# Kernel optimization log

Measured on AMD Instinct MI355X. Metric: run time of the kernel, lower is better.

The kernel has to match this reference:

```python
import jax, jax.numpy as jnp
import numpy as np

# dims: batch, query grid len, key (irregular obs) len, raw features, time-embed dim, heads
B, TQ, TK, F, ET, H = 8, 48, 128, 64, 64, 8
DK = ET // H          # per-head time-embed dim = 8
D = 2 * F             # attention value dim = cat(X, mask) = 128
NEG = -10000.0        # masked_fill constant from the torch code


def setup_inputs() -> dict:
    key = jax.random.key(0)
    ks = jax.random.split(key, 12)
    X = jax.random.normal(ks[0], (B, TK, F), dtype=jnp.float32)
    mask_X = (jax.random.uniform(ks[1], (B, TK, F)) < 0.7).astype(jnp.float32)
    T = jax.random.uniform(ks[2], (B, TK), dtype=jnp.float32) * 48.0
    alpha = jax.random.uniform(ks[3], (B, TQ), dtype=jnp.float32) * 48.0
    s = 0.05
    # time embedding params: linear(1->1) and periodic(1 -> ET-1)
    w_lin = jax.random.normal(ks[4], (1, 1)) * s
    b_lin = jnp.zeros((1,), jnp.float32)
    w_per = jax.random.normal(ks[5], (1, ET - 1)) * s
    b_per = jnp.zeros((ET - 1,), jnp.float32)
    # attention projections (stored as [in, out], i.e. torch weight transposed)
    Wq = jax.random.normal(ks[6], (ET, ET)) * s
    bq = jnp.zeros((ET,), jnp.float32)
    Wk = jax.random.normal(ks[7], (ET, ET)) * s
    bk = jnp.zeros((ET,), jnp.float32)
    Wo = jax.random.normal(ks[8], (H * D, ET)) * s   # nhidden = embed_time = ET
    bo = jnp.zeros((ET,), jnp.float32)
    return {"X": X, "mask_X": mask_X, "T": T, "alpha": alpha,
            "w_lin": w_lin, "b_lin": b_lin, "w_per": w_per, "b_per": b_per,
            "Wq": Wq, "bq": bq, "Wk": Wk, "bk": bk, "Wo": Wo, "bo": bo}


def _time_embed(t, w_lin, b_lin, w_per, b_per):
    # t: [B, L] -> [B, L, ET]; cat(linear(t), sin(periodic(t)))
    t = t[..., None]
    return jnp.concatenate([t @ w_lin + b_lin, jnp.sin(t @ w_per + b_per)], axis=-1)


def reference(X, mask_X, T, alpha, w_lin, b_lin, w_per, b_per,
              Wq, bq, Wk, bk, Wo, bo):
    # mTAND core (eval mode, dropout off)
    keys = _time_embed(T, w_lin, b_lin, w_per, b_per)        # [B, TK, ET]
    query = _time_embed(alpha, w_lin, b_lin, w_per, b_per)   # [B, TQ, ET]
    X_irg = jnp.concatenate([X, mask_X], axis=-1)            # [B, TK, D]
    M = jnp.concatenate([mask_X, mask_X], axis=-1)           # [B, TK, D]

    q = (query @ Wq + bq).reshape(B, TQ, H, DK).transpose(0, 2, 1, 3)  # [B,H,TQ,DK]
    k = (keys @ Wk + bk).reshape(B, TK, H, DK).transpose(0, 2, 1, 3)   # [B,H,TK,DK]

    scores = jnp.einsum('bhqd,bhkd->bhqk', q, k) / (DK ** 0.5)        # [B,H,TQ,TK]
    # expand per value-channel and masked_fill(-10000) where mask == 0
    logits = jnp.where(M[:, None, None, :, :] == 0, NEG, scores[..., None])  # [B,H,TQ,TK,D]
    p_attn = jax.nn.softmax(logits, axis=-2)                            # softmax over TK
    out = jnp.einsum('bhqkd,bkd->bhqd', p_attn, X_irg)                  # [B,H,TQ,D]

    x = out.transpose(0, 2, 1, 3).reshape(B, TQ, H * D)                 # [B,TQ,H*D]
    return x @ Wo + bo                                                  # [B,TQ,ET]
```

## Files before the change

kernel.cpp:

```cpp
#include <hip/hip_runtime.h>
#include <math.h>

#define B   8
#define TQ  48
#define TK  128
#define F   64
#define ET  64
#define H   8
#define DK  8
#define D   128

__global__ __launch_bounds__(256) void embed_proj_kernel(
    const float* __restrict__ T,
    const float* __restrict__ alpha,
    const float* __restrict__ w_lin, const float* __restrict__ b_lin,
    const float* __restrict__ w_per, const float* __restrict__ b_per,
    const float* __restrict__ Wq, const float* __restrict__ bq,
    const float* __restrict__ Wk, const float* __restrict__ bk,
    float* __restrict__ kws,
    float* __restrict__ qws)
{
    __shared__ float es[4][ET];
    const int tid = threadIdx.x;
    const int rl  = tid >> 6;
    const int o   = tid & 63;
    const int row = blockIdx.x * 4 + rl;

    const bool is_key = row < B * TK;
    const float t = is_key ? T[row] : alpha[row - B * TK];

    float e;
    if (o == 0) e = t * w_lin[0] + b_lin[0];
    else        e = sinf(t * w_per[o - 1] + b_per[o - 1]);
    es[rl][o] = e;
    __syncthreads();

    const float* Wp   = is_key ? Wk : Wq;
    const float* bias = is_key ? bk : bq;
    float acc = bias[o];
    #pragma unroll 8
    for (int i = 0; i < ET; ++i)
        acc = fmaf(es[rl][i], Wp[i * ET + o], acc);

    if (is_key) {
        const int b  = row >> 7;
        const int kk = row & 127;
        const int h  = o >> 3;
        const int dk = o & 7;
        kws[((b * H + h) * TK + kk) * DK + dk] = acc;
    } else {
        const int r = row - B * TK;
        qws[r * ET + o] = acc;
    }
}

__global__ __launch_bounds__(512) void attn_kernel(
    const float* __restrict__ X,
    const float* __restrict__ mask,
    const float* __restrict__ kws,
    const float* __restrict__ qws,
    const float* __restrict__ Wo,
    const float* __restrict__ bo,
    float* __restrict__ out)
{
    __shared__ float qs[ET];
    __shared__ float Es[H][TK];
    __shared__ float maxs[H];
    __shared__ float Xs[TK][F];
    __shared__ unsigned long long Mb[TK];
    __shared__ float xs[H * D];
    __shared__ float pden[4][H * F];
    __shared__ float pnum[4][H * F];
    __shared__ float red[32][ET];

    const int tid = threadIdx.x;
    const int b = blockIdx.x / TQ;
    const int q = blockIdx.x % TQ;

    if (tid < ET) qs[tid] = qws[(b * TQ + q) * ET + tid];

    const float4* X4  = (const float4*)(X + b * TK * F);
    float4*       Xs4 = (float4*)&Xs[0][0];
    #pragma unroll
    for (int i = 0; i < 4; ++i)
        Xs4[tid + 512 * i] = X4[tid + 512 * i];

    {
        const int wave = tid >> 6, lane = tid & 63;
        const float* mrow = mask + b * TK * F;
        #pragma unroll 4
        for (int i = 0; i < 16; ++i) {
            const int kk = wave * 16 + i;
            const unsigned long long bal = __ballot(mrow[kk * F + lane] != 0.0f);
            if (lane == 0) Mb[kk] = bal;
        }
    }
    __syncthreads();

    const float4* k4 = (const float4*)(kws + b * H * TK * DK);
    #pragma unroll
    for (int i = 0; i < 2; ++i) {
        const int p = tid + 512 * i;
        const int h = p >> 7, kk = p & 127;
        const float4 a0 = k4[(h * TK + kk) * 2 + 0];
        const float4 a1 = k4[(h * TK + kk) * 2 + 1];
        const float* qh = &qs[h * DK];
        float s = a0.x * qh[0] + a0.y * qh[1] + a0.z * qh[2] + a0.w * qh[3]
                + a1.x * qh[4] + a1.y * qh[5] + a1.z * qh[6] + a1.w * qh[7];
        Es[h][kk] = s * 0.35355339059327373f;
    }
    __syncthreads();

    if (tid < 256) {
        const int h = tid >> 5, j = tid & 31;
        float m = fmaxf(fmaxf(Es[h][j], Es[h][j + 32]),
                        fmaxf(Es[h][j + 64], Es[h][j + 96]));
        #pragma unroll
        for (int dlt = 16; dlt >= 1; dlt >>= 1)
            m = fmaxf(m, __shfl_xor(m, dlt));
        if (j == 0) maxs[h] = m;
    }
    __syncthreads();

    #pragma unroll
    for (int i = 0; i < 2; ++i) {
        const int p = tid + 512 * i;
        const int h = p >> 7, kk = p & 127;
        Es[h][kk] = expf(Es[h][kk] - maxs[h]);
    }
    __syncthreads();

    {
        const int f4 = (tid & 15) * 4;
        const int h  = (tid >> 4) & 7;
        const int ks = tid >> 7;
        const int k0 = ks * 32;
        float d0 = 0, d1 = 0, d2 = 0, d3 = 0;
        float n0 = 0, n1 = 0, n2 = 0, n3 = 0;
        #pragma unroll 8
        for (int i = 0; i < 32; ++i) {
            const int kk = k0 + i;
            const float e  = Es[h][kk];
            const float4 x = *(const float4*)&Xs[kk][f4];
            const unsigned int mb = (unsigned int)(Mb[kk] >> f4);
            const float e0 = (mb & 1u) ? e : 0.0f;
            const float e1 = (mb & 2u) ? e : 0.0f;
            const float e2 = (mb & 4u) ? e : 0.0f;
            const float e3 = (mb & 8u) ? e : 0.0f;
            d0 += e0; d1 += e1; d2 += e2; d3 += e3;
            n0 = fmaf(e0, x.x, n0); n1 = fmaf(e1, x.y, n1);
            n2 = fmaf(e2, x.z, n2); n3 = fmaf(e3, x.w, n3);
        }
        const int base = h * F + f4;
        *(float4*)&pden[ks][base] = make_float4(d0, d1, d2, d3);
        *(float4*)&pnum[ks][base] = make_float4(n0, n1, n2, n3);
    }
    __syncthreads();

    {
        const int h = tid >> 6, f = tid & 63;
        const int idx = h * F + f;
        const float den = pden[0][idx] + pden[1][idx] + pden[2][idx] + pden[3][idx];
        const float num = pnum[0][idx] + pnum[1][idx] + pnum[2][idx] + pnum[3][idx];
        float outX, outM;
        if (den > 0.0f) {
            outX = num / den;
            outM = 1.0f;
        } else {
            float sX = 0.0f;
            for (int kk = 0; kk < TK; ++kk) sX += Xs[kk][f];
            outX = sX * (1.0f / TK);
            outM = 0.0f;
        }
        xs[h * D + f]      = outX;
        xs[h * D + 64 + f] = outM;
    }
    __syncthreads();

    {
        const int e4 = (tid & 15) * 4;
        const int p  = tid >> 4;
        const int j0 = p * 32;
        float ax = 0, ay = 0, az = 0, aw = 0;
        #pragma unroll 8
        for (int i = 0; i < 32; ++i) {
            const int j = j0 + i;
            const float xj = xs[j];
            const float4 w = *(const float4*)&Wo[j * ET + e4];
            ax = fmaf(xj, w.x, ax); ay = fmaf(xj, w.y, ay);
            az = fmaf(xj, w.z, az); aw = fmaf(xj, w.w, aw);
        }
        *(float4*)&red[p][e4] = make_float4(ax, ay, az, aw);
    }
    __syncthreads();
    if (tid < ET) {
        float acc = bo[tid];
        #pragma unroll
        for (int p = 0; p < 32; ++p) acc += red[p][tid];
        out[(b * TQ + q) * ET + tid] = acc;
    }
}

extern "C" void kernel_launch(void* const* d_in, const int* in_sizes, int n_in,
                              void* d_out, int out_size, void* d_ws, size_t ws_size,
                              hipStream_t stream) {
    const float* X      = (const float*)d_in[0];
    const float* mask_X = (const float*)d_in[1];
    const float* T      = (const float*)d_in[2];
    const float* alpha  = (const float*)d_in[3];
    const float* w_lin  = (const float*)d_in[4];
    const float* b_lin  = (const float*)d_in[5];
    const float* w_per  = (const float*)d_in[6];
    const float* b_per  = (const float*)d_in[7];
    const float* Wq     = (const float*)d_in[8];
    const float* bq     = (const float*)d_in[9];
    const float* Wk     = (const float*)d_in[10];
    const float* bk     = (const float*)d_in[11];
    const float* Wo     = (const float*)d_in[12];
    const float* bo     = (const float*)d_in[13];
    float* out = (float*)d_out;

    float* kws = (float*)d_ws;
    float* qws = kws + B * H * TK * DK;

    embed_proj_kernel<<<dim3((B * TK + B * TQ) / 4), dim3(256), 0, stream>>>(
        T, alpha, w_lin, b_lin, w_per, b_per, Wq, bq, Wk, bk, kws, qws);

    attn_kernel<<<dim3(B * TQ), dim3(512), 0, stream>>>(
        X, mask_X, kws, qws, Wo, bo, out);
}
```

Baseline: 100.9 us.

## Restructure attention block: per-wave head scores, drop X smem staging, merge syncs

Each wave now owns one head: it computes scores for all 128 keys in registers, does the max with a wave-wide shuffle and writes exp values into a key-major [TK][H] shared array. This removes the separate max and exp phases and their barriers. X is no longer staged in shared memory; each thread reads its column straight from global memory and accumulates all 8 heads at once, with partial sums reduced over 8 wave slices as float2 pairs. Fewer barriers and less LDS traffic are traded for more scattered global X reads and more registers per thread.

Result: no change. 99.12 us (-1.7%).

```diff
diff --git a/kernel.cpp b/kernel.cpp
--- a/kernel.cpp
+++ b/kernel.cpp
@@ -63,30 +63,18 @@
     const float* __restrict__ bo,
     float* __restrict__ out)
 {
-    __shared__ float qs[ET];
-    __shared__ float Es[H][TK];
-    __shared__ float maxs[H];
-    __shared__ float Xs[TK][F];
+    __shared__ float Est[TK][H];
     __shared__ unsigned long long Mb[TK];
+    __shared__ float2 pdn[8][H][F];
     __shared__ float xs[H * D];
-    __shared__ float pden[4][H * F];
-    __shared__ float pnum[4][H * F];
     __shared__ float red[32][ET];
 
-    const int tid = threadIdx.x;
+    const int tid  = threadIdx.x;
+    const int wave = tid >> 6, lane = tid & 63;
     const int b = blockIdx.x / TQ;
     const int q = blockIdx.x % TQ;
 
-    if (tid < ET) qs[tid] = qws[(b * TQ + q) * ET + tid];
-
-    const float4* X4  = (const float4*)(X + b * TK * F);
-    float4*       Xs4 = (float4*)&Xs[0][0];
-    #pragma unroll
-    for (int i = 0; i < 4; ++i)
-        Xs4[tid + 512 * i] = X4[tid + 512 * i];
-
-    {
-        const int wave = tid >> 6, lane = tid & 63;
+    {
         const float* mrow = mask + b * TK * F;
         #pragma unroll 4
         for (int i = 0; i < 16; ++i) {
@@ -94,81 +82,78 @@
             const unsigned long long bal = __ballot(mrow[kk * F + lane] != 0.0f);
             if (lane == 0) Mb[kk] = bal;
         }
-    }
-    __syncthreads();
-
-    const float4* k4 = (const float4*)(kws + b * H * TK * DK);
-    #pragma unroll
-    for (int i = 0; i < 2; ++i) {
-        const int p = tid + 512 * i;
-        const int h = p >> 7, kk = p & 127;
-        const float4 a0 = k4[(h * TK + kk) * 2 + 0];
-        const float4 a1 = k4[(h * TK + kk) * 2 + 1];
-        const float* qh = &qs[h * DK];
-        float s = a0.x * qh[0] + a0.y * qh[1] + a0.z * qh[2] + a0.w * qh[3]
-                + a1.x * qh[4] + a1.y * qh[5] + a1.z * qh[6] + a1.w * qh[7];
-        Es[h][kk] = s * 0.35355339059327373f;
-    }
-    __syncthreads();
-
-    if (tid < 256) {
-        const int h = tid >> 5, j = tid & 31;
-        float m = fmaxf(fmaxf(Es[h][j], Es[h][j + 32]),
-                        fmaxf(Es[h][j + 64], Es[h][j + 96]));
-        #pragma unroll
-        for (int dlt = 16; dlt >= 1; dlt >>= 1)
+
+        const float* qrow = qws + (b * TQ + q) * ET + wave * DK;
+        float qh[8];
+        #pragma unroll
+        for (int d = 0; d < 8; ++d) qh[d] = qrow[d];
+
+        const float4* k4 = (const float4*)(kws + (b * H + wave) * TK * DK);
+        const float4 a0 = k4[lane * 2 + 0];
+        const float4 a1 = k4[lane * 2 + 1];
+        const float4 c0 = k4[(lane + 64) * 2 + 0];
+        const float4 c1 = k4[(lane + 64) * 2 + 1];
+        const float inv = 0.35355339059327373f;
+        float s0 = (a0.x*qh[0] + a0.y*qh[1] + a0.z*qh[2] + a0.w*qh[3]
+                  + a1.x*qh[4] + a1.y*qh[5] + a1.z*qh[6] + a1.w*qh[7]) * inv;
+        float s1 = (c0.x*qh[0] + c0.y*qh[1] + c0.z*qh[2] + c0.w*qh[3]
+                  + c1.x*qh[4] + c1.y*qh[5] + c1.z*qh[6] + c1.w*qh[7]) * inv;
+
+        float m = fmaxf(s0, s1);
+        #pragma unroll
+        for (int dlt = 32; dlt >= 1; dlt >>= 1)
             m = fmaxf(m, __shfl_xor(m, dlt));
-        if (j == 0) maxs[h] = m;
-    }
-    __syncthreads();
-
-    #pragma unroll
-    for (int i = 0; i < 2; ++i) {
-        const int p = tid + 512 * i;
-        const int h = p >> 7, kk = p & 127;
-        Es[h][kk] = expf(Es[h][kk] - maxs[h]);
-    }
-    __syncthreads();
-
-    {
-        const int f4 = (tid & 15) * 4;
-        const int h  = (tid >> 4) & 7;
-        const int ks = tid >> 7;
-        const int k0 = ks * 32;
-        float d0 = 0, d1 = 0, d2 = 0, d3 = 0;
-        float n0 = 0, n1 = 0, n2 = 0, n3 = 0;
-        #pragma unroll 8
-        for (int i = 0; i < 32; ++i) {
+
+        Est[lane][wave]      = expf(s0 - m);
+        Est[lane + 64][wave] = expf(s1 - m);
+    }
+    __syncthreads();
+
+    {
+        const int f = lane;
+        const float* Xrow = X + b * TK * F + f;
+        float den[8], num[8];
+        #pragma unroll
+        for (int h = 0; h < 8; ++h) { den[h] = 0.0f; num[h] = 0.0f; }
+        const int k0 = wave * 16;
+        #pragma unroll 4
+        for (int i = 0; i < 16; ++i) {
             const int kk = k0 + i;
-            const float e  = Es[h][kk];
-            const float4 x = *(const float4*)&Xs[kk][f4];
-            const unsigned int mb = (unsigned int)(Mb[kk] >> f4);
-            const float e0 = (mb & 1u) ? e : 0.0f;
-            const float e1 = (mb & 2u) ? e : 0.0f;
-            const float e2 = (mb & 4u) ? e : 0.0f;
-            const float e3 = (mb & 8u) ? e : 0.0f;
-            d0 += e0; d1 += e1; d2 += e2; d3 += e3;
-            n0 = fmaf(e0, x.x, n0); n1 = fmaf(e1, x.y, n1);
-            n2 = fmaf(e2, x.z, n2); n3 = fmaf(e3, x.w, n3);
-        }
-        const int base = h * F + f4;
-        *(float4*)&pden[ks][base] = make_float4(d0, d1, d2, d3);
-        *(float4*)&pnum[ks][base] = make_float4(n0, n1, n2, n3);
-    }
-    __syncthreads();
-
-    {
-        const int h = tid >> 6, f = tid & 63;
-        const int idx = h * F + f;
-        const float den = pden[0][idx] + pden[1][idx] + pden[2][idx] + pden[3][idx];
-        const float num = pnum[0][idx] + pnum[1][idx] + pnum[2][idx] + pnum[3][idx];
+            const float x = Xrow[kk * F];
+            const unsigned int bit = (unsigned int)(Mb[kk] >> f) & 1u;
+            const float4 e0 = *(const float4*)&Est[kk][0];
+            const float4 e1 = *(const float4*)&Est[kk][4];
+            const float ev[8] = {e0.x, e0.y, e0.z, e0.w,
+                                 e1.x, e1.y, e1.z, e1.w};
+            #pragma unroll
+            for (int h = 0; h < 8; ++h) {
+                const float em = bit ? ev[h] : 0.0f;
+                den[h] += em;
+                num[h] = fmaf(em, x, num[h]);
+            }
+        }
+        #pragma unroll
+        for (int h = 0; h < 8; ++h)
+            pdn[wave][h][f] = make_float2(den[h], num[h]);
+    }
+    __syncthreads();
+
+    {
+        const int h = wave, f = lane;
+        float den = 0.0f, num = 0.0f;
+        #pragma unroll
+        for (int ks = 0; ks < 8; ++ks) {
+            const float2 v = pdn[ks][h][f];
+            den += v.x; num += v.y;
+        }
         float outX, outM;
         if (den > 0.0f) {
             outX = num / den;
             outM = 1.0f;
         } else {
+            const float* Xrow = X + b * TK * F + f;
             float sX = 0.0f;
-            for (int kk = 0; kk < TK; ++kk) sX += Xs[kk][f];
+            for (int kk = 0; kk < TK; ++kk) sX += Xrow[kk * F];
             outX = sX * (1.0f / TK);
             outM = 0.0f;
         }
@@ -193,6 +178,7 @@
         *(float4*)&red[p][e4] = make_float4(ax, ay, az, aw);
     }
     __syncthreads();
+
     if (tid < ET) {
         float acc = bo[tid];
         #pragma unroll
```
